# Kernel tuning notes

Hardware: AMD Instinct MI355X
Metric: run time of the kernel (lower is better)

Reference implementation:

```python
import jax, jax.numpy as jnp
import numpy as np

N_EMBD = 1024
N_HEAD = 16
HEAD_DIM = N_EMBD // N_HEAD


def setup_inputs() -> dict:
    key = jax.random.key(0)
    ks = jax.random.split(key, 9)
    B, T, C = 2, 2048, N_EMBD
    s = 1.0 / np.sqrt(C)
    inp = {
        "x": jax.random.normal(ks[0], (B, T, C), dtype=jnp.float32),
        "Wq": jax.random.normal(ks[1], (C, C), dtype=jnp.float32) * s,
        "bq": jnp.zeros((C,), dtype=jnp.float32),
        "Wk": jax.random.normal(ks[2], (C, C), dtype=jnp.float32) * s,
        "bk": jnp.zeros((C,), dtype=jnp.float32),
        "Wv": jax.random.normal(ks[3], (C, C), dtype=jnp.float32) * s,
        "bv": jnp.zeros((C,), dtype=jnp.float32),
        "Wo": jax.random.normal(ks[4], (C, C), dtype=jnp.float32) * s,
        "bo": jnp.zeros((C,), dtype=jnp.float32),
    }
    return inp


def reference(x, Wq, bq, Wk, bk, Wv, bv, Wo, bo):
    B, T, C = x.shape
    H, D = N_HEAD, HEAD_DIM
    # projections (torch Linear: x @ W^T + b)
    q = (x @ Wq.T + bq).reshape(B, T, H, D).transpose(0, 2, 1, 3)  # [B,H,T,D]
    k = (x @ Wk.T + bk).reshape(B, T, H, D).transpose(0, 2, 1, 3)
    v = (x @ Wv.T + bv).reshape(B, T, H, D).transpose(0, 2, 1, 3)
    scores = jnp.einsum("bhqd,bhkd->bhqk", q, k) / jnp.sqrt(jnp.asarray(D, x.dtype))
    causal = jnp.tril(jnp.ones((T, T), dtype=bool))
    scores = jnp.where(causal[None, None], scores, jnp.asarray(-jnp.inf, x.dtype))
    weights = jax.nn.softmax(scores, axis=-1)  # [B,H,T,T]
    attended = jnp.einsum("bhqk,bhkd->bhqd", weights, v)
    attended = attended.transpose(0, 2, 1, 3).reshape(B, T, C)
    return attended @ Wo.T + bo
```

## Files before the change

### kernel.cpp

```cpp
#include <hip/hip_runtime.h>

typedef unsigned short u16;
typedef __attribute__((ext_vector_type(8))) __bf16 bf16x8;
typedef __attribute__((ext_vector_type(4))) float f32x4;
typedef __attribute__((ext_vector_type(4))) unsigned int u32x4;

#define MFMA16(a, b, c) __builtin_amdgcn_mfma_f32_16x16x32_bf16(a, b, c, 0, 0, 0)

__device__ __forceinline__ u16 f2bf(float f) {
    unsigned u = __float_as_uint(f);
    u = (u + 0x7FFFu + ((u >> 16) & 1u)) >> 16;
    return (u16)u;
}

__device__ __forceinline__ void gl_lds16(const u16* g, u16* l) {
    __builtin_amdgcn_global_load_lds(
        (const __attribute__((address_space(1))) unsigned int*)g,
        (__attribute__((address_space(3))) unsigned int*)l, 16, 0, 0);
}

static constexpr int Bv = 2, Tv = 2048, Cv = 1024, Hv = 16, Dv = 64;
static constexpr int Mv = Bv * Tv;

static constexpr size_t OFF_XB = 0;
static constexpr size_t OFF_WQ = 4194304;
static constexpr size_t OFF_WK = OFF_WQ + 1048576;
static constexpr size_t OFF_WV = OFF_WK + 1048576;
static constexpr size_t OFF_WO = OFF_WV + 1048576;
static constexpr size_t OFF_Q  = OFF_WO + 1048576;
static constexpr size_t OFF_K  = OFF_Q + 4194304;
static constexpr size_t OFF_VT = OFF_K + 4194304;
static constexpr size_t OFF_A  = OFF_VT + 4194304;

__global__ __launch_bounds__(256) void convert_all(
    const float* __restrict__ x,
    const float* __restrict__ wq, const float* __restrict__ wk,
    const float* __restrict__ wv, const float* __restrict__ wo,
    u16* __restrict__ dst)
{
    int i4 = blockIdx.x * blockDim.x + threadIdx.x;
    if (i4 >= 2097152) return;
    int idx = i4 * 4;
    const float* src; int off;
    if (idx < 4194304) { src = x; off = idx; }
    else {
        int rel = idx - 4194304;
        int j = rel >> 20;
        off = rel & 1048575;
        src = (j == 0) ? wq : (j == 1) ? wk : (j == 2) ? wv : wo;
    }
    float4 v = *(const float4*)(src + off);
    ushort4 o;
    o.x = f2bf(v.x); o.y = f2bf(v.y); o.z = f2bf(v.z); o.w = f2bf(v.w);
    *(ushort4*)(dst + idx) = o;
}

template <bool OUT_BF16, bool ROWBIAS>
__device__ __forceinline__ void gemm128_b64(
    const u16* __restrict__ A, const u16* __restrict__ Wt,
    const float* __restrict__ bias, void* __restrict__ outp,
    int m0, int n0, int N, int K)
{
    __shared__ u16 lA[128 * 64];
    __shared__ u16 lB[128 * 64];
    const int tid  = threadIdx.x;
    const int lane = tid & 63, w = tid >> 6;
    const int quad = lane >> 4, lm = lane & 15;
    const int wm = (w & 1) * 64, wn = (w >> 1) * 64;

    f32x4 zero = {0.f, 0.f, 0.f, 0.f};
    f32x4 acc[4][4];
    #pragma unroll
    for (int mt = 0; mt < 4; mt++)
        #pragma unroll
        for (int nt = 0; nt < 4; nt++) acc[mt][nt] = zero;

    const int rowi = lane >> 3, seg = lane & 7;

    for (int k0 = 0; k0 < K; k0 += 64) {
        #pragma unroll
        for (int i = 0; i < 4; i++) {
            int rbase = w * 32 + i * 8;
            int row = rbase + rowi;
            int gseg = seg ^ (row & 7);
            gl_lds16(A  + (size_t)(m0 + row) * K + k0 + gseg * 8, &lA[rbase * 64]);
            gl_lds16(Wt + (size_t)(n0 + row) * K + k0 + gseg * 8, &lB[rbase * 64]);
        }
        __syncthreads();
        #pragma unroll
        for (int ks = 0; ks < 2; ks++) {
            const int swz = ((ks * 4 + quad) ^ (lm & 7)) * 8;
            bf16x8 af[4], bf[4];
            #pragma unroll
            for (int mt = 0; mt < 4; mt++)
                af[mt] = *(const bf16x8*)&lA[(wm + mt * 16 + lm) * 64 + swz];
            #pragma unroll
            for (int nt = 0; nt < 4; nt++)
                bf[nt] = *(const bf16x8*)&lB[(wn + nt * 16 + lm) * 64 + swz];
            #pragma unroll
            for (int mt = 0; mt < 4; mt++)
                #pragma unroll
                for (int nt = 0; nt < 4; nt++)
                    acc[mt][nt] = MFMA16(af[mt], bf[nt], acc[mt][nt]);
        }
        __syncthreads();
    }

    #pragma unroll
    for (int nt = 0; nt < 4; nt++) {
        int col = n0 + wn + nt * 16 + lm;
        float cb = ROWBIAS ? 0.f : bias[col];
        #pragma unroll
        for (int mt = 0; mt < 4; mt++) {
            #pragma unroll
            for (int r = 0; r < 4; r++) {
                int row = m0 + wm + mt * 16 + quad * 4 + r;
                float v = acc[mt][nt][r] + (ROWBIAS ? bias[row] : cb);
                if (OUT_BF16) ((u16*)outp)[(size_t)row * N + col] = f2bf(v);
                else          ((float*)outp)[(size_t)row * N + col] = v;
            }
        }
    }
}

__global__ __launch_bounds__(256) void gemm_qkv(
    const u16* __restrict__ A,
    const u16* __restrict__ Wq, const u16* __restrict__ Wk, const u16* __restrict__ Wv,
    const float* __restrict__ bq, const float* __restrict__ bk, const float* __restrict__ bv,
    u16* __restrict__ Q, u16* __restrict__ K, u16* __restrict__ VT)
{
    int nb = blockIdx.x;
    int which = nb >> 3;
    if (which == 0) {
        gemm128_b64<true, false>(A, Wq, bq, Q, blockIdx.y * 128, (nb & 7) * 128, Cv, Cv);
    } else if (which == 1) {
        gemm128_b64<true, false>(A, Wk, bk, K, blockIdx.y * 128, (nb & 7) * 128, Cv, Cv);
    } else {
        gemm128_b64<true, true>(Wv, A, bv, VT, (nb & 7) * 128, blockIdx.y * 128, Mv, Cv);
    }
}

__global__ __launch_bounds__(256) void gemm_o64(
    const u16* __restrict__ A, const u16* __restrict__ Wt,
    const float* __restrict__ bias, float* __restrict__ outp)
{
    __shared__ u16 lA[128 * 64];
    __shared__ u16 lB[64 * 64];
    const int tid  = threadIdx.x;
    const int lane = tid & 63, w = tid >> 6;
    const int quad = lane >> 4, lm = lane & 15;
    const int m0 = blockIdx.y * 128, n0 = blockIdx.x * 64;
    const int K = Cv;

    f32x4 zero = {0.f, 0.f, 0.f, 0.f};
    f32x4 acc[2][4];
    #pragma unroll
    for (int mt = 0; mt < 2; mt++)
        #pragma unroll
        for (int nt = 0; nt < 4; nt++) acc[mt][nt] = zero;

    const int rowi = lane >> 3, seg = lane & 7;

    for (int k0 = 0; k0 < K; k0 += 64) {
        #pragma unroll
        for (int i = 0; i < 4; i++) {
            int rbase = w * 32 + i * 8;
            int row = rbase + rowi;
            int gseg = seg ^ (row & 7);
            gl_lds16(A + (size_t)(m0 + row) * K + k0 + gseg * 8, &lA[rbase * 64]);
        }
        {
            int rbase = w * 16, row0 = rbase + rowi, row1 = row0 + 8;
            gl_lds16(Wt + (size_t)(n0 + row0) * K + k0 + (seg ^ (row0 & 7)) * 8, &lB[rbase * 64]);
            gl_lds16(Wt + (size_t)(n0 + row1) * K + k0 + (seg ^ (row1 & 7)) * 8, &lB[(rbase + 8) * 64]);
        }
        __syncthreads();
        #pragma unroll
        for (int ks = 0; ks < 2; ks++) {
            const int swz = ((ks * 4 + quad) ^ (lm & 7)) * 8;
            bf16x8 af[2], bf[4];
            #pragma unroll
            for (int mt = 0; mt < 2; mt++)
                af[mt] = *(const bf16x8*)&lA[(w * 32 + mt * 16 + lm) * 64 + swz];
            #pragma unroll
            for (int nt = 0; nt < 4; nt++)
                bf[nt] = *(const bf16x8*)&lB[(nt * 16 + lm) * 64 + swz];
            #pragma unroll
            for (int mt = 0; mt < 2; mt++)
                #pragma unroll
                for (int nt = 0; nt < 4; nt++)
                    acc[mt][nt] = MFMA16(af[mt], bf[nt], acc[mt][nt]);
        }
        __syncthreads();
    }

    #pragma unroll
    for (int nt = 0; nt < 4; nt++) {
        int col = n0 + nt * 16 + lm;
        float bvv = bias[col];
        #pragma unroll
        for (int mt = 0; mt < 2; mt++) {
            #pragma unroll
            for (int r = 0; r < 4; r++) {
                int row = m0 + w * 32 + mt * 16 + quad * 4 + r;
                outp[(size_t)row * Cv + col] = acc[mt][nt][r] + bvv;
            }
        }
    }
}

__global__ __launch_bounds__(256) void attn(
    const u16* __restrict__ Qp, const u16* __restrict__ Kp,
    const u16* __restrict__ VTg, u16* __restrict__ Op)
{
    __shared__ u16 lK[2][64 * 64];
    __shared__ u16 lVT[2][64 * 64];
    __shared__ u16 lP[4][32][72];

    const int tid  = threadIdx.x;
    const int lane = tid & 63, w = tid >> 6;
    const int quad = lane >> 4, lm = lane & 15;

    const int idx  = blockIdx.x;
    const int half = idx >> 8;
    const int grp  = idx & 255;
    const int bh   = grp >> 3;
    const int j    = grp & 7;
    const int qt   = half ? j : 15 - j;
    const int h = bh & 15, b = bh >> 4;

    const int qb = qt * 128;
    const size_t headoff = (size_t)b * Tv * Cv + (size_t)h * Dv;
    const size_t vthead  = (size_t)h * 64 * Mv + (size_t)b * Tv;

    bf16x8 qf[2][2];
    #pragma unroll
    for (int nt = 0; nt < 2; nt++) {
        const u16* qptr = Qp + headoff + (size_t)(qb + w * 32 + nt * 16 + lm) * Cv + quad * 8;
        qf[0][nt] = *(const bf16x8*)(qptr);
        qf[1][nt] = *(const bf16x8*)(qptr + 32);
    }

    f32x4 zero = {0.f, 0.f, 0.f, 0.f};
    f32x4 oacc[2][4];
    #pragma unroll
    for (int mt = 0; mt < 2; mt++)
        #pragma unroll
        for (int nt = 0; nt < 4; nt++) oacc[mt][nt] = zero;
    float Lp[2] = {0.f, 0.f};

    const float SC = 0.18033688011112042f;
    const int rowi = lane >> 3, seg = lane & 7;
    const int niter = qt * 2 + 2;

    auto stage = [&](int bsel, int kt) {
        const int k0 = kt * 64;
        #pragma unroll
        for (int hf = 0; hf < 2; hf++) {
            int rbase = w * 16 + hf * 8;
            int row = rbase + rowi;
            int gseg = seg ^ (row & 7);
            gl_lds16(Kp + headoff + (size_t)(k0 + row) * Cv + gseg * 8, &lK[bsel][rbase * 64]);
            gl_lds16(VTg + vthead + (size_t)row * Mv + k0 + gseg * 8, &lVT[bsel][rbase * 64]);
        }
    };

    stage(0, 0);

    for (int kt = 0; kt < niter; kt++) {
        const int bsel = kt & 1;
        const int k0 = kt * 64;
        __syncthreads();
        if (kt + 1 < niter) stage(bsel ^ 1, kt + 1);

        f32x4 stt[4][2];
        #pragma unroll
        for (int mt = 0; mt < 4; mt++)
            #pragma unroll
            for (int nt = 0; nt < 2; nt++) stt[mt][nt] = zero;
        #pragma unroll
        for (int ks = 0; ks < 2; ks++) {
            #pragma unroll
            for (int mt = 0; mt < 4; mt++) {
                bf16x8 kf = *(const bf16x8*)
                    &lK[bsel][(mt * 16 + lm) * 64 + (((ks * 4 + quad) ^ (lm & 7)) * 8)];
                #pragma unroll
                for (int nt = 0; nt < 2; nt++)
                    stt[mt][nt] = MFMA16(kf, qf[ks][nt], stt[mt][nt]);
            }
        }

        const bool needmask = (kt >= niter - 2);
        #pragma unroll
        for (int mt = 0; mt < 4; mt++) {
            #pragma unroll
            for (int nt = 0; nt < 2; nt++) {
                const int keyb = k0 + mt * 16 + quad * 4;
                const int qrow = qb + w * 32 + nt * 16 + lm;
                ushort4 pk;
                float e0 = __builtin_amdgcn_exp2f(fmaf(stt[mt][nt][0], SC, -16.f));
                float e1 = __builtin_amdgcn_exp2f(fmaf(stt[mt][nt][1], SC, -16.f));
                float e2 = __builtin_amdgcn_exp2f(fmaf(stt[mt][nt][2], SC, -16.f));
                float e3 = __builtin_amdgcn_exp2f(fmaf(stt[mt][nt][3], SC, -16.f));
                if (needmask) {
                    if (keyb + 0 > qrow) e0 = 0.f;
                    if (keyb + 1 > qrow) e1 = 0.f;
                    if (keyb + 2 > qrow) e2 = 0.f;
                    if (keyb + 3 > qrow) e3 = 0.f;
                }
                Lp[nt] += e0 + e1 + e2 + e3;
                pk.x = (u16)(__float_as_uint(e0) >> 16);
                pk.y = (u16)(__float_as_uint(e1) >> 16);
                pk.z = (u16)(__float_as_uint(e2) >> 16);
                pk.w = (u16)(__float_as_uint(e3) >> 16);
                *(ushort4*)&lP[w][nt * 16 + lm][mt * 16 + quad * 4] = pk;
            }
        }

        #pragma unroll
        for (int ks = 0; ks < 2; ks++) {
            bf16x8 pf[2];
            #pragma unroll
            for (int mt = 0; mt < 2; mt++)
                pf[mt] = *(const bf16x8*)&lP[w][mt * 16 + lm][ks * 32 + quad * 8];
            #pragma unroll
            for (int nt = 0; nt < 4; nt++) {
                bf16x8 vf = *(const bf16x8*)
                    &lVT[bsel][(nt * 16 + lm) * 64 + (((ks * 4 + quad) ^ (lm & 7)) * 8)];
                #pragma unroll
                for (int mt = 0; mt < 2; mt++)
                    oacc[mt][nt] = MFMA16(pf[mt], vf, oacc[mt][nt]);
            }
        }
    }

    float Lred[2];
    #pragma unroll
    for (int nt = 0; nt < 2; nt++) {
        float L = Lp[nt];
        L += __shfl_xor(L, 16, 64);
        L += __shfl_xor(L, 32, 64);
        Lred[nt] = 1.0f / L;
    }
    #pragma unroll
    for (int mt = 0; mt < 2; mt++) {
        float inv[4];
        #pragma unroll
        for (int r = 0; r < 4; r++)
            inv[r] = __shfl(Lred[mt], (lane & 48) | (quad * 4 + r), 64);
        #pragma unroll
        for (int nt = 0; nt < 4; nt++) {
            #pragma unroll
            for (int r = 0; r < 4; r++) {
                int row = qb + w * 32 + mt * 16 + quad * 4 + r;
                Op[headoff + (size_t)row * Cv + nt * 16 + lm] = f2bf(oacc[mt][nt][r] * inv[r]);
            }
        }
    }
}

extern "C" void kernel_launch(void* const* d_in, const int* in_sizes, int n_in,
                              void* d_out, int out_size, void* d_ws, size_t ws_size,
                              hipStream_t stream) {
    const float* x  = (const float*)d_in[0];
    const float* Wq = (const float*)d_in[1];
    const float* bq = (const float*)d_in[2];
    const float* Wk = (const float*)d_in[3];
    const float* bk = (const float*)d_in[4];
    const float* Wv = (const float*)d_in[5];
    const float* bv = (const float*)d_in[6];
    const float* Wo = (const float*)d_in[7];
    const float* bo = (const float*)d_in[8];
    u16* ws = (u16*)d_ws;

    convert_all<<<8192, 256, 0, stream>>>(x, Wq, Wk, Wv, Wo, ws);

    gemm_qkv<<<dim3(24, 32), 256, 0, stream>>>(
        ws + OFF_XB, ws + OFF_WQ, ws + OFF_WK, ws + OFF_WV,
        bq, bk, bv, ws + OFF_Q, ws + OFF_K, ws + OFF_VT);

    attn<<<512, 256, 0, stream>>>(ws + OFF_Q, ws + OFF_K, ws + OFF_VT, ws + OFF_A);

    gemm_o64<<<dim3(16, 32), 256, 0, stream>>>(ws + OFF_A, ws + OFF_WO, bo, (float*)d_out);
}
```

Before: 196.4 us.

## Split attention key tiles across two wave groups per block and merge in LDS

The attention block grows to 512 threads as two groups of four waves. The groups take alternating 64-key tiles for the same 128 queries, and their partial outputs and row sums are combined through LDS at the end. This halves the serial key-loop length per block and raises the waves per block. In exchange it drops the double-buffered prefetch, so every tile now does load, sync, then compute with no overlap. It also adds a reduction pass through LDS and changes the block-to-(head, query-tile) mapping.

```diff
diff --git a/kernel.cpp b/kernel.cpp
--- a/kernel.cpp
+++ b/kernel.cpp
@@ -209,23 +209,24 @@
     }
 }
 
-__global__ __launch_bounds__(256) void attn(
+__global__ __launch_bounds__(512) void attn(
     const u16* __restrict__ Qp, const u16* __restrict__ Kp,
     const u16* __restrict__ VTg, u16* __restrict__ Op)
 {
     __shared__ u16 lK[2][64 * 64];
     __shared__ u16 lVT[2][64 * 64];
-    __shared__ u16 lP[4][32][72];
+    __shared__ u16 lP[8][32][72];
 
     const int tid  = threadIdx.x;
     const int lane = tid & 63, w = tid >> 6;
+    const int g = w >> 2, wl = w & 3;
     const int quad = lane >> 4, lm = lane & 15;
 
     const int idx  = blockIdx.x;
     const int half = idx >> 8;
     const int grp  = idx & 255;
-    const int bh   = grp >> 3;
-    const int j    = grp & 7;
+    const int bh   = (half << 4) | (grp >> 4);
+    const int j    = grp & 15;
     const int qt   = half ? j : 15 - j;
     const int h = bh & 15, b = bh >> 4;
 
@@ -236,7 +237,7 @@
     bf16x8 qf[2][2];
     #pragma unroll
     for (int nt = 0; nt < 2; nt++) {
-        const u16* qptr = Qp + headoff + (size_t)(qb + w * 32 + nt * 16 + lm) * Cv + quad * 8;
+        const u16* qptr = Qp + headoff + (size_t)(qb + wl * 32 + nt * 16 + lm) * Cv + quad * 8;
         qf[0][nt] = *(const bf16x8*)(qptr);
         qf[1][nt] = *(const bf16x8*)(qptr + 32);
     }
@@ -251,28 +252,21 @@
 
     const float SC = 0.18033688011112042f;
     const int rowi = lane >> 3, seg = lane & 7;
-    const int niter = qt * 2 + 2;
-
-    auto stage = [&](int bsel, int kt) {
+
+    auto stage = [&](int kt) {
         const int k0 = kt * 64;
         #pragma unroll
         for (int hf = 0; hf < 2; hf++) {
-            int rbase = w * 16 + hf * 8;
+            int rbase = wl * 16 + hf * 8;
             int row = rbase + rowi;
             int gseg = seg ^ (row & 7);
-            gl_lds16(Kp + headoff + (size_t)(k0 + row) * Cv + gseg * 8, &lK[bsel][rbase * 64]);
-            gl_lds16(VTg + vthead + (size_t)row * Mv + k0 + gseg * 8, &lVT[bsel][rbase * 64]);
+            gl_lds16(Kp + headoff + (size_t)(k0 + row) * Cv + gseg * 8, &lK[g][rbase * 64]);
+            gl_lds16(VTg + vthead + (size_t)row * Mv + k0 + gseg * 8, &lVT[g][rbase * 64]);
         }
     };
 
-    stage(0, 0);
-
-    for (int kt = 0; kt < niter; kt++) {
-        const int bsel = kt & 1;
+    auto body = [&](int kt, bool domask) __attribute__((always_inline)) {
         const int k0 = kt * 64;
-        __syncthreads();
-        if (kt + 1 < niter) stage(bsel ^ 1, kt + 1);
-
         f32x4 stt[4][2];
         #pragma unroll
         for (int mt = 0; mt < 4; mt++)
@@ -283,32 +277,30 @@
             #pragma unroll
             for (int mt = 0; mt < 4; mt++) {
                 bf16x8 kf = *(const bf16x8*)
-                    &lK[bsel][(mt * 16 + lm) * 64 + (((ks * 4 + quad) ^ (lm & 7)) * 8)];
+                    &lK[g][(mt * 16 + lm) * 64 + (((ks * 4 + quad) ^ (lm & 7)) * 8)];
                 #pragma unroll
                 for (int nt = 0; nt < 2; nt++)
                     stt[mt][nt] = MFMA16(kf, qf[ks][nt], stt[mt][nt]);
             }
         }
-
-        const bool needmask = (kt >= niter - 2);
         #pragma unroll
         for (int mt = 0; mt < 4; mt++) {
             #pragma unroll
             for (int nt = 0; nt < 2; nt++) {
                 const int keyb = k0 + mt * 16 + quad * 4;
-                const int qrow = qb + w * 32 + nt * 16 + lm;
-                ushort4 pk;
+                const int qrow = qb + wl * 32 + nt * 16 + lm;
                 float e0 = __builtin_amdgcn_exp2f(fmaf(stt[mt][nt][0], SC, -16.f));
                 float e1 = __builtin_amdgcn_exp2f(fmaf(stt[mt][nt][1], SC, -16.f));
                 float e2 = __builtin_amdgcn_exp2f(fmaf(stt[mt][nt][2], SC, -16.f));
                 float e3 = __builtin_amdgcn_exp2f(fmaf(stt[mt][nt][3], SC, -16.f));
-                if (needmask) {
+                if (domask) {
                     if (keyb + 0 > qrow) e0 = 0.f;
                     if (keyb + 1 > qrow) e1 = 0.f;
                     if (keyb + 2 > qrow) e2 = 0.f;
                     if (keyb + 3 > qrow) e3 = 0.f;
                 }
                 Lp[nt] += e0 + e1 + e2 + e3;
+                ushort4 pk;
                 pk.x = (u16)(__float_as_uint(e0) >> 16);
                 pk.y = (u16)(__float_as_uint(e1) >> 16);
                 pk.z = (u16)(__float_as_uint(e2) >> 16);
@@ -316,7 +308,6 @@
                 *(ushort4*)&lP[w][nt * 16 + lm][mt * 16 + quad * 4] = pk;
             }
         }
-
         #pragma unroll
         for (int ks = 0; ks < 2; ks++) {
             bf16x8 pf[2];
@@ -326,34 +317,73 @@
             #pragma unroll
             for (int nt = 0; nt < 4; nt++) {
                 bf16x8 vf = *(const bf16x8*)
-                    &lVT[bsel][(nt * 16 + lm) * 64 + (((ks * 4 + quad) ^ (lm & 7)) * 8)];
+                    &lVT[g][(nt * 16 + lm) * 64 + (((ks * 4 + quad) ^ (lm & 7)) * 8)];
                 #pragma unroll
                 for (int mt = 0; mt < 2; mt++)
                     oacc[mt][nt] = MFMA16(pf[mt], vf, oacc[mt][nt]);
             }
         }
-    }
-
-    float Lred[2];
-    #pragma unroll
-    for (int nt = 0; nt < 2; nt++) {
-        float L = Lp[nt];
-        L += __shfl_xor(L, 16, 64);
-        L += __shfl_xor(L, 32, 64);
-        Lred[nt] = 1.0f / L;
-    }
-    #pragma unroll
-    for (int mt = 0; mt < 2; mt++) {
-        float inv[4];
-        #pragma unroll
-        for (int r = 0; r < 4; r++)
-            inv[r] = __shfl(Lred[mt], (lane & 48) | (quad * 4 + r), 64);
-        #pragma unroll
-        for (int nt = 0; nt < 4; nt++) {
-            #pragma unroll
-            for (int r = 0; r < 4; r++) {
-                int row = qb + w * 32 + mt * 16 + quad * 4 + r;
-                Op[headoff + (size_t)row * Cv + nt * 16 + lm] = f2bf(oacc[mt][nt][r] * inv[r]);
+    };
+
+    for (int i = 0; i < qt; i++) {
+        if (i) __syncthreads();
+        stage(2 * i + g);
+        __syncthreads();
+        body(2 * i + g, false);
+    }
+    if (qt) __syncthreads();
+    stage(2 * qt + g);
+    __syncthreads();
+    body(2 * qt + g, true);
+    __syncthreads();
+
+    float* lO = (float*)&lP[0][0][0];
+    float* lL = lO + 32 * 256;
+    const int t = tid & 255;
+    if (g == 1) {
+        #pragma unroll
+        for (int mt = 0; mt < 2; mt++)
+            #pragma unroll
+            for (int nt = 0; nt < 4; nt++)
+                #pragma unroll
+                for (int r = 0; r < 4; r++)
+                    lO[(mt * 16 + nt * 4 + r) * 256 + t] = oacc[mt][nt][r];
+        lL[t] = Lp[0];
+        lL[256 + t] = Lp[1];
+    }
+    __syncthreads();
+    if (g == 0) {
+        #pragma unroll
+        for (int mt = 0; mt < 2; mt++)
+            #pragma unroll
+            for (int nt = 0; nt < 4; nt++)
+                #pragma unroll
+                for (int r = 0; r < 4; r++)
+                    oacc[mt][nt][r] += lO[(mt * 16 + nt * 4 + r) * 256 + t];
+        Lp[0] += lL[t];
+        Lp[1] += lL[256 + t];
+
+        float Lred[2];
+        #pragma unroll
+        for (int nt = 0; nt < 2; nt++) {
+            float L = Lp[nt];
+            L += __shfl_xor(L, 16, 64);
+            L += __shfl_xor(L, 32, 64);
+            Lred[nt] = 1.0f / L;
+        }
+        #pragma unroll
+        for (int mt = 0; mt < 2; mt++) {
+            float inv[4];
+            #pragma unroll
+            for (int r = 0; r < 4; r++)
+                inv[r] = __shfl(Lred[mt], (lane & 48) | (quad * 4 + r), 64);
+            #pragma unroll
+            for (int nt = 0; nt < 4; nt++) {
+                #pragma unroll
+                for (int r = 0; r < 4; r++) {
+                    int row = qb + wl * 32 + mt * 16 + quad * 4 + r;
+                    Op[headoff + (size_t)row * Cv + nt * 16 + lm] = f2bf(oacc[mt][nt][r] * inv[r]);
+                }
             }
         }
     }
@@ -379,7 +409,7 @@
         ws + OFF_XB, ws + OFF_WQ, ws + OFF_WK, ws + OFF_WV,
         bq, bk, bv, ws + OFF_Q, ws + OFF_K, ws + OFF_VT);
 
-    attn<<<512, 256, 0, stream>>>(ws + OFF_Q, ws + OFF_K, ws + OFF_VT, ws + OFF_A);
+    attn<<<512, 512, 0, stream>>>(ws + OFF_Q, ws + OFF_K, ws + OFF_VT, ws + OFF_A);
 
     gemm_o64<<<dim3(16, 32), 256, 0, stream>>>(ws + OFF_A, ws + OFF_WO, bo, (float*)d_out);
 }
```

Measured after the change: 182.1 us. 1.08x faster.
